# Kernel tuning notes

Measured on AMD Instinct MI355X. Metric: run time of the kernel, lower is better.

The kernel has to match this reference:

```python
import jax, jax.numpy as jnp
import numpy as np

N_NODES = 100000
HIDDEN = 128


def _gcn_conv(x, edge_index, W, b, n_nodes):
    # PyG GCNConv with default symmetric normalization and self-loops.
    src, dst = edge_index[0], edge_index[1]
    loop = jnp.arange(n_nodes, dtype=src.dtype)
    src = jnp.concatenate([src, loop])
    dst = jnp.concatenate([dst, loop])
    # degree over destination nodes (edge weight = 1), self-loops included
    deg = jax.ops.segment_sum(jnp.ones_like(dst, dtype=x.dtype), dst,
                              num_segments=n_nodes)
    dinv = jax.lax.rsqrt(deg)  # deg >= 1 because of self-loops
    norm = dinv[src] * dinv[dst]  # [E+N]
    h = x @ W  # [N, 4H] linear transform first (d_in -> 4H)
    msg = norm[:, None] * h[src]  # [E+N, 4H]
    out = jax.ops.segment_sum(msg, dst, num_segments=n_nodes)
    return out + b


def setup_inputs() -> dict:
    key = jax.random.key(0)
    k1, k2, k3, k4, k5, k6 = jax.random.split(key, 6)
    n, h = N_NODES, HIDDEN
    x = jax.random.normal(k1, (n, h), dtype=jnp.float32)
    h_cur = jax.random.normal(k2, (n, h), dtype=jnp.float32)
    c_cur = jax.random.normal(k3, (n, h), dtype=jnp.float32)
    edge_index = jax.random.randint(k4, (2, 3200000), 0, n, dtype=jnp.int64)
    W = jax.random.normal(k5, (h, 4 * h), dtype=jnp.float32) / np.sqrt(h)
    b = jax.random.normal(k6, (4 * h,), dtype=jnp.float32) * 0.01
    return {"x": x, "edge_index": edge_index, "h_cur": h_cur,
            "c_cur": c_cur, "W": W, "b": b}


def reference(x, edge_index, h_cur, c_cur, W, b):
    combined = x + h_cur  # fused input + hidden add
    conv = _gcn_conv(combined, edge_index, W, b, x.shape[0])  # [N, 4H]
    cc_f = conv[:, :HIDDEN]  # first gate chunk (module returns cc_f only)
    return cc_f
```

## Files before the change

### kernel.cpp

```cpp
#include <hip/hip_runtime.h>
#include <hip/hip_bf16.h>

#define HID 128
#define NGR_SH 7
#define MAXGRP 1024
#define NSB 256
#define CAPG 4608

__device__ __forceinline__ float b2f(unsigned short u) {
    union { unsigned i; float f; } v; v.i = ((unsigned)u) << 16; return v.f;
}
__device__ __forceinline__ unsigned short f2b(float f) {
    unsigned u = __float_as_uint(f);
    return (unsigned short)((u + 0x7fffu + ((u >> 16) & 1u)) >> 16);
}

__global__ __launch_bounds__(256) void histgemm_kernel(const int* __restrict__ ei,
                                                       unsigned* __restrict__ hist,
                                                       const float* __restrict__ x,
                                                       const float* __restrict__ hc,
                                                       const float* __restrict__ W,
                                                       unsigned short* __restrict__ hp,
                                                       int E, int n, int ngroups) {
    __shared__ union {
        unsigned h[MAXGRP];
        float A[64 * 132];
    } sm;
    int tid = threadIdx.x;

    if (blockIdx.x < NSB) {
        for (int g = tid; g < ngroups; g += 256) sm.h[g] = 0u;
        __syncthreads();
        int chunk = (E + NSB - 1) / NSB;
        int beg = blockIdx.x * chunk, end = min(E, beg + chunk);
        for (int i = beg + tid; i < end; i += 256) {
            int dst = ei[(size_t)E + i];
            if ((unsigned)dst < (unsigned)n) atomicAdd(&sm.h[dst >> NGR_SH], 1u);
        }
        __syncthreads();
        for (int g = tid; g < ngroups; g += 256)
            hist[(size_t)blockIdx.x * ngroups + g] = sm.h[g];
    } else {
        int r0 = (blockIdx.x - NSB) * 64;
        for (int i = tid; i < 2048; i += 256) {
            int row = i >> 5;
            int c4 = (i & 31) * 4;
            int grow = r0 + row;
            float4 v;
            if (grow < n) {
                float4 a = *(const float4*)(x + (size_t)grow * HID + c4);
                float4 bb = *(const float4*)(hc + (size_t)grow * HID + c4);
                v = make_float4(a.x + bb.x, a.y + bb.y, a.z + bb.z, a.w + bb.w);
            } else {
                v = make_float4(0.f, 0.f, 0.f, 0.f);
            }
            *(float4*)(&sm.A[row * 132 + c4]) = v;
        }
        __syncthreads();

        int cg = tid & 31;
        int c4 = cg * 4;
        int rg = tid >> 5;
        float acc[8][4];
#pragma unroll
        for (int r = 0; r < 8; ++r) {
            acc[r][0] = 0.f; acc[r][1] = 0.f; acc[r][2] = 0.f; acc[r][3] = 0.f;
        }
#pragma unroll 4
        for (int k = 0; k < 128; ++k) {
            float4 w = *(const float4*)(W + (size_t)k * 512 + c4);
#pragma unroll
            for (int r = 0; r < 8; ++r) {
                float a = sm.A[(rg * 8 + r) * 132 + k];
                acc[r][0] += a * w.x;
                acc[r][1] += a * w.y;
                acc[r][2] += a * w.z;
                acc[r][3] += a * w.w;
            }
        }
#pragma unroll
        for (int r = 0; r < 8; ++r) {
            int grow = r0 + rg * 8 + r;
            if (grow < n) {
                unsigned long long pack =
                    (unsigned long long)f2b(acc[r][0]) |
                    ((unsigned long long)f2b(acc[r][1]) << 16) |
                    ((unsigned long long)f2b(acc[r][2]) << 32) |
                    ((unsigned long long)f2b(acc[r][3]) << 48);
                *(unsigned long long*)(hp + (size_t)grow * HID + c4) = pack;
            }
        }
    }
}

__global__ __launch_bounds__(256) void scan2d_kernel(const unsigned* __restrict__ hist,
                                                     unsigned* __restrict__ base_rel,
                                                     unsigned* __restrict__ gcount,
                                                     int ngroups) {
    int g = blockIdx.x;
    int t = threadIdx.x;
    unsigned v = hist[(size_t)t * ngroups + g];
    int lane = t & 63, w = t >> 6;
    unsigned x = v;
    for (int d = 1; d < 64; d <<= 1) {
        unsigned y = __shfl_up(x, d, 64);
        if (lane >= d) x += y;
    }
    __shared__ unsigned wsum[4];
    if (lane == 63) wsum[w] = x;
    __syncthreads();
    unsigned add = 0;
    for (int ww = 0; ww < 4; ++ww) if (ww < w) add += wsum[ww];
    unsigned incl = x + add;
    base_rel[(size_t)t * ngroups + g] = incl - v;
    if (t == 255) gcount[g] = incl;
}

__global__ __launch_bounds__(1024) void gscan_kernel(const unsigned* __restrict__ gcount,
                                                     unsigned* __restrict__ gboff,
                                                     int ngroups) {
    __shared__ unsigned sums[1024];
    int t = threadIdx.x;
    int chunk = (ngroups + 1023) >> 10;
    int beg = min(t * chunk, ngroups), end = min(beg + chunk, ngroups);
    unsigned local = 0;
    for (int i = beg; i < end; ++i) local += gcount[i];
    sums[t] = local;
    __syncthreads();
    for (int d = 1; d < 1024; d <<= 1) {
        unsigned v = (t >= d) ? sums[t - d] : 0u;
        __syncthreads();
        sums[t] += v;
        __syncthreads();
    }
    unsigned run = (t > 0) ? sums[t - 1] : 0u;
    for (int i = beg; i < end; ++i) { gboff[i] = run; run += gcount[i]; }
    if (t == 1023) gboff[ngroups] = sums[1023];
}

__global__ __launch_bounds__(256) void gscatter_kernel(const int* __restrict__ ei,
                                                       const unsigned* __restrict__ gboff,
                                                       const unsigned* __restrict__ base_rel,
                                                       unsigned* __restrict__ grouped,
                                                       int E, int n, int ngroups) {
    __shared__ unsigned cursor[MAXGRP];
    int blk = blockIdx.x;
    int tid = threadIdx.x;
    for (int g = tid; g < ngroups; g += 256)
        cursor[g] = gboff[g] + base_rel[(size_t)blk * ngroups + g];
    __syncthreads();
    int chunk = (E + NSB - 1) / NSB;
    int beg = blk * chunk, end = min(E, beg + chunk);
    for (int i = beg + tid; i < end; i += 256) {
        int s = ei[i];
        int dst = ei[(size_t)E + i];
        if ((unsigned)dst >= (unsigned)n) continue;
        unsigned ss = (unsigned)min(max(s, 0), n - 1);
        unsigned slot = atomicAdd(&cursor[dst >> NGR_SH], 1u);
        grouped[slot] = ss | ((unsigned)(dst & ((1 << NGR_SH) - 1)) << 17);
    }
}

__global__ __launch_bounds__(256) void dinvg_kernel(const unsigned* __restrict__ grouped,
                                                    const unsigned* __restrict__ gboff,
                                                    float* __restrict__ dinv, int n) {
    __shared__ unsigned lcnt[128];
    int g = blockIdx.x;
    int t = threadIdx.x;
    if (t < 128) lcnt[t] = 0u;
    __syncthreads();
    unsigned s0 = gboff[g], s1 = gboff[g + 1];
    for (unsigned j = s0 + t; j < s1; j += 256) atomicAdd(&lcnt[grouped[j] >> 17], 1u);
    __syncthreads();
    if (t < 128) {
        int node = (g << NGR_SH) + t;
        if (node < n) dinv[node] = rsqrtf((float)(lcnt[t] + 1u));
    }
}

__global__ __launch_bounds__(512) void aggsort_kernel(const unsigned* __restrict__ grouped,
                                                      const unsigned* __restrict__ gboff,
                                                      const float* __restrict__ dinv,
                                                      const unsigned short* __restrict__ hp,
                                                      const float* __restrict__ bias,
                                                      float* __restrict__ out, int n) {
    __shared__ unsigned srcs_lds[CAPG];
    __shared__ unsigned nodeoff[129];
    __shared__ unsigned cursor[128];
    __shared__ float sdinv[128];
    __shared__ unsigned wtot[2];
    int g = blockIdx.x;
    int tid = threadIdx.x;
    unsigned s0 = gboff[g], s1 = gboff[g + 1];
    unsigned cnt = s1 - s0;
    int node0 = g << NGR_SH;

    if (tid < 128) {
        int node = node0 + tid;
        sdinv[tid] = (node < n) ? dinv[node] : 0.f;
        cursor[tid] = 0u;
    }
    __syncthreads();

    if (cnt <= CAPG) {
        for (unsigned j = s0 + tid; j < s1; j += 512) atomicAdd(&cursor[grouped[j] >> 17], 1u);
        __syncthreads();
        unsigned v = 0, xsc = 0;
        if (tid < 128) {
            v = cursor[tid];
            xsc = v;
            int lane = tid & 63;
            for (int d = 1; d < 64; d <<= 1) {
                unsigned y = __shfl_up(xsc, d, 64);
                if (lane >= d) xsc += y;
            }
            if (lane == 63) wtot[tid >> 6] = xsc;
        }
        __syncthreads();
        if (tid < 128) {
            unsigned excl = xsc - v + ((tid >= 64) ? wtot[0] : 0u);
            nodeoff[tid] = excl;
            cursor[tid] = excl;
            if (tid == 127) nodeoff[128] = cnt;
        }
        __syncthreads();
        for (unsigned j = s0 + tid; j < s1; j += 512) {
            unsigned p = grouped[j];
            unsigned slot = atomicAdd(&cursor[p >> 17], 1u);
            srcs_lds[slot] = p & 0x1FFFFu;
        }
        __syncthreads();

        int w = tid >> 6, lane = tid & 63;
        int c = lane * 2;
        for (int nl = w * 16; nl < w * 16 + 16; ++nl) {
            int node = node0 + nl;
            if (node >= n) break;
            unsigned beg = nodeoff[nl], end2 = nodeoff[nl + 1];
            float ax = 0.f, ay = 0.f;
            unsigned i = beg;
            for (; i + 8 <= end2; i += 8) {
                unsigned s[8]; float wd[8]; ushort2 v2[8];
#pragma unroll
                for (int j = 0; j < 8; ++j) s[j] = srcs_lds[i + j];
#pragma unroll
                for (int j = 0; j < 8; ++j) wd[j] = dinv[s[j]];
#pragma unroll
                for (int j = 0; j < 8; ++j) v2[j] = *(const ushort2*)(hp + ((size_t)s[j] << 7) + c);
#pragma unroll
                for (int j = 0; j < 8; ++j) { ax += wd[j] * b2f(v2[j].x); ay += wd[j] * b2f(v2[j].y); }
            }
            if (i < end2) {
                unsigned last = end2 - 1;
                unsigned s[8]; float wd[8]; ushort2 v2[8];
#pragma unroll
                for (int j = 0; j < 8; ++j) {
                    unsigned jj = i + j;
                    s[j] = srcs_lds[jj < end2 ? jj : last];
                    wd[j] = (jj < end2) ? 1.f : 0.f;
                }
#pragma unroll
                for (int j = 0; j < 8; ++j) wd[j] *= dinv[s[j]];
#pragma unroll
                for (int j = 0; j < 8; ++j) v2[j] = *(const ushort2*)(hp + ((size_t)s[j] << 7) + c);
#pragma unroll
                for (int j = 0; j < 8; ++j) { ax += wd[j] * b2f(v2[j].x); ay += wd[j] * b2f(v2[j].y); }
            }
            float dd = sdinv[nl];
            ushort2 hd = *(const ushort2*)(hp + ((size_t)node << 7) + c);
            ax += dd * b2f(hd.x);
            ay += dd * b2f(hd.y);
            float2 bb = *(const float2*)(bias + c);
            float2 res = make_float2(dd * ax + bb.x, dd * ay + bb.y);
            *(float2*)(out + ((size_t)node << 7) + c) = res;
        }
    } else {
        for (int idx = tid; idx < 128 * HID; idx += 512) {
            int ndl = idx >> 7, col = idx & (HID - 1);
            int node = node0 + ndl;
            if (node < n) {
                float dd = sdinv[ndl];
                out[((size_t)node << 7) + col] = dd * dd * b2f(hp[((size_t)node << 7) + col]) + bias[col];
            }
        }
        __syncthreads();
        if (tid < 64) {
            int c = tid * 2;
            for (unsigned j = s0; j < s1; ++j) {
                unsigned p = grouped[j];
                unsigned dl = p >> 17, s = p & 0x1FFFFu;
                float wsc = dinv[s] * sdinv[dl];
                ushort2 v = *(const ushort2*)(hp + ((size_t)s << 7) + c);
                float2* o = (float2*)(out + ((size_t)(node0 + dl) << 7) + c);
                float2 cur = *o;
                cur.x += wsc * b2f(v.x);
                cur.y += wsc * b2f(v.y);
                *o = cur;
            }
        }
    }
}

extern "C" void kernel_launch(void* const* d_in, const int* in_sizes, int n_in,
                              void* d_out, int out_size, void* d_ws, size_t ws_size,
                              hipStream_t stream) {
    const float* x = (const float*)d_in[0];
    const int* ei = (const int*)d_in[1];
    const float* hc = (const float*)d_in[2];
    const float* W = (const float*)d_in[4];
    const float* b = (const float*)d_in[5];
    float* out = (float*)d_out;

    int n = in_sizes[0] / HID;
    int E = in_sizes[1] / 2;
    int ngroups = (n + 127) >> NGR_SH;

    char* ws = (char*)d_ws;
    unsigned* gcount = (unsigned*)(ws);
    unsigned* gboff  = (unsigned*)(ws + 8192);
    float*    dinv   = (float*)   (ws + 16384);
    unsigned* grouped= (unsigned*)(ws + 416384);
    unsigned short* hp = (unsigned short*)(ws + 13216384);

    unsigned* hist     = (unsigned*)d_out;
    unsigned* base_rel = hist + (size_t)NSB * ngroups;

    int gemm_blocks = (n + 63) / 64;
    histgemm_kernel<<<NSB + gemm_blocks, 256, 0, stream>>>(ei, hist, x, hc, W, hp, E, n, ngroups);
    scan2d_kernel<<<ngroups, 256, 0, stream>>>(hist, base_rel, gcount, ngroups);
    gscan_kernel<<<1, 1024, 0, stream>>>(gcount, gboff, ngroups);
    gscatter_kernel<<<NSB, 256, 0, stream>>>(ei, gboff, base_rel, grouped, E, n, ngroups);
    dinvg_kernel<<<ngroups, 256, 0, stream>>>(grouped, gboff, dinv, n);
    aggsort_kernel<<<ngroups, 512, 0, stream>>>(grouped, gboff, dinv, hp, b, out, n);
}
```

Baseline: 261.2 us.

## Split each aggregation group across two 256-thread blocks by node half

The aggregation kernel now launches two blocks per 128-node group, each owning 64 destination nodes and filtering the group's edges by a half bit. Each block holds a smaller LDS source buffer and runs 256 threads, which is meant to raise occupancy and spread work across more CUs. The cost is that both blocks read the full group edge list twice, once to count and once to scatter. The per-group capacity check now applies per half.

```diff
diff --git a/kernel.cpp b/kernel.cpp
--- a/kernel.cpp
+++ b/kernel.cpp
@@ -5,7 +5,7 @@
 #define NGR_SH 7
 #define MAXGRP 1024
 #define NSB 256
-#define CAPG 4608
+#define CAPH 2560
 
 __device__ __forceinline__ float b2f(unsigned short u) {
     union { unsigned i; float f; } v; v.i = ((unsigned)u) << 16; return v.f;
@@ -178,56 +178,57 @@
     }
 }
 
-__global__ __launch_bounds__(512) void aggsort_kernel(const unsigned* __restrict__ grouped,
+__global__ __launch_bounds__(256) void aggsort_kernel(const unsigned* __restrict__ grouped,
                                                       const unsigned* __restrict__ gboff,
                                                       const float* __restrict__ dinv,
                                                       const unsigned short* __restrict__ hp,
                                                       const float* __restrict__ bias,
                                                       float* __restrict__ out, int n) {
-    __shared__ unsigned srcs_lds[CAPG];
-    __shared__ unsigned nodeoff[129];
-    __shared__ unsigned cursor[128];
-    __shared__ float sdinv[128];
-    __shared__ unsigned wtot[2];
-    int g = blockIdx.x;
+    __shared__ unsigned srcs_lds[CAPH];
+    __shared__ unsigned nodeoff[65];
+    __shared__ unsigned cursor[64];
+    __shared__ float sdinv[64];
+    int blk = blockIdx.x;
+    unsigned half = blk & 1u;
+    int g = blk >> 1;
     int tid = threadIdx.x;
     unsigned s0 = gboff[g], s1 = gboff[g + 1];
-    unsigned cnt = s1 - s0;
-    int node0 = g << NGR_SH;
-
-    if (tid < 128) {
+    int node0 = (g << NGR_SH) + (int)half * 64;
+
+    if (tid < 64) {
         int node = node0 + tid;
         sdinv[tid] = (node < n) ? dinv[node] : 0.f;
         cursor[tid] = 0u;
     }
     __syncthreads();
 
-    if (cnt <= CAPG) {
-        for (unsigned j = s0 + tid; j < s1; j += 512) atomicAdd(&cursor[grouped[j] >> 17], 1u);
-        __syncthreads();
-        unsigned v = 0, xsc = 0;
-        if (tid < 128) {
-            v = cursor[tid];
-            xsc = v;
-            int lane = tid & 63;
-            for (int d = 1; d < 64; d <<= 1) {
-                unsigned y = __shfl_up(xsc, d, 64);
-                if (lane >= d) xsc += y;
-            }
-            if (lane == 63) wtot[tid >> 6] = xsc;
-        }
-        __syncthreads();
-        if (tid < 128) {
-            unsigned excl = xsc - v + ((tid >= 64) ? wtot[0] : 0u);
-            nodeoff[tid] = excl;
-            cursor[tid] = excl;
-            if (tid == 127) nodeoff[128] = cnt;
-        }
-        __syncthreads();
-        for (unsigned j = s0 + tid; j < s1; j += 512) {
+    for (unsigned j = s0 + tid; j < s1; j += 256) {
+        unsigned p = grouped[j];
+        if (((p >> 23) & 1u) == half) atomicAdd(&cursor[(p >> 17) & 63u], 1u);
+    }
+    __syncthreads();
+    if (tid < 64) {
+        unsigned v = cursor[tid];
+        unsigned x = v;
+        for (int d = 1; d < 64; d <<= 1) {
+            unsigned y = __shfl_up(x, d, 64);
+            if (tid >= d) x += y;
+        }
+        unsigned excl = x - v;
+        nodeoff[tid] = excl;
+        cursor[tid] = excl;
+        if (tid == 63) nodeoff[64] = x;
+    }
+    __syncthreads();
+    unsigned hcnt = nodeoff[64];
+
+    if (hcnt <= CAPH) {
+        for (unsigned j = s0 + tid; j < s1; j += 256) {
             unsigned p = grouped[j];
-            unsigned slot = atomicAdd(&cursor[p >> 17], 1u);
-            srcs_lds[slot] = p & 0x1FFFFu;
+            if (((p >> 23) & 1u) == half) {
+                unsigned slot = atomicAdd(&cursor[(p >> 17) & 63u], 1u);
+                srcs_lds[slot] = p & 0x1FFFFu;
+            }
         }
         __syncthreads();
 
@@ -275,7 +276,7 @@
             *(float2*)(out + ((size_t)node << 7) + c) = res;
         }
     } else {
-        for (int idx = tid; idx < 128 * HID; idx += 512) {
+        for (int idx = tid; idx < 64 * HID; idx += 256) {
             int ndl = idx >> 7, col = idx & (HID - 1);
             int node = node0 + ndl;
             if (node < n) {
@@ -288,10 +289,13 @@
             int c = tid * 2;
             for (unsigned j = s0; j < s1; ++j) {
                 unsigned p = grouped[j];
-                unsigned dl = p >> 17, s = p & 0x1FFFFu;
+                if (((p >> 23) & 1u) != half) continue;
+                unsigned dl = (p >> 17) & 63u, s = p & 0x1FFFFu;
+                int node = node0 + (int)dl;
+                if (node >= n) continue;
                 float wsc = dinv[s] * sdinv[dl];
                 ushort2 v = *(const ushort2*)(hp + ((size_t)s << 7) + c);
-                float2* o = (float2*)(out + ((size_t)(node0 + dl) << 7) + c);
+                float2* o = (float2*)(out + ((size_t)node << 7) + c);
                 float2 cur = *o;
                 cur.x += wsc * b2f(v.x);
                 cur.y += wsc * b2f(v.y);
@@ -331,5 +335,5 @@
     gscan_kernel<<<1, 1024, 0, stream>>>(gcount, gboff, ngroups);
     gscatter_kernel<<<NSB, 256, 0, stream>>>(ei, gboff, base_rel, grouped, E, n, ngroups);
     dinvg_kernel<<<ngroups, 256, 0, stream>>>(grouped, gboff, dinv, n);
-    aggsort_kernel<<<ngroups, 512, 0, stream>>>(grouped, gboff, dinv, hp, b, out, n);
-}
+    aggsort_kernel<<<ngroups * 2, 256, 0, stream>>>(grouped, gboff, dinv, hp, b, out, n);
+}
```

Result: faster. 252.0 us (-3.5%).
